# Performance work log

Hardware: AMD Instinct MI355X
Metric: run time of the kernel (lower is better)

Reference implementation:

```python
import jax, jax.numpy as jnp
import numpy as np

B, N, M, K = 8, 24000, 6000, 32
C_IN, C_MID, C_OUT = 64, 128, 256  # channels=[64,128,256]; conv input is C_IN+3 (dp_fj)


def setup_inputs() -> dict:
    key = jax.random.key(0)
    ks = jax.random.split(key, 8)
    return {
        "query_xyz": jax.random.normal(ks[0], (B, M, 3), jnp.float32),
        "support_xyz": jax.random.normal(ks[1], (B, N, 3), jnp.float32),
        "features": jax.random.normal(ks[2], (B, C_IN, N), jnp.float32),
        "neighbor_idx": jax.random.randint(ks[3], (B, M, K), 0, N, dtype=jnp.int32),
        "W1": jax.random.normal(ks[4], (C_MID, C_IN + 3), jnp.float32) * 0.05,
        "b1": jnp.zeros((C_MID,), jnp.float32),
        "W2": jax.random.normal(ks[5], (C_OUT, C_MID), jnp.float32) * 0.05,
        "b2": jnp.zeros((C_OUT,), jnp.float32),
    }


def _conv1d_relu(x, W, b):
    # pointwise conv1d (kernel size 1) + bias + ReLU; x: [B, Cin, N]
    return jax.nn.relu(jnp.einsum('oc,bcn->bon', W, x) + b[None, :, None])


def reference(query_xyz, support_xyz, features, neighbor_idx, W1, b1, W2, b2):
    # Delayed aggregation: transform features FIRST (convs on support points),
    # then gather neighbors per query and max-reduce.
    x = jnp.concatenate([features, support_xyz.transpose(0, 2, 1)], axis=1)  # [B, C_IN+3, N]
    x = _conv1d_relu(x, W1, b1)   # [B, C_MID, N]
    x = _conv1d_relu(x, W2, b2)   # [B, C_OUT, N]
    # grouper: gather neighbor features fj = x[b, :, neighbor_idx[b, m, k]] -> [B, C_OUT, M, K]
    idx = jnp.broadcast_to(neighbor_idx.reshape(B, 1, M * K), (B, C_OUT, M * K))
    fj = jnp.take_along_axis(x, idx, axis=2).reshape(B, C_OUT, M, K)
    # reduction_layer: max over neighbor dim
    return jnp.max(fj, axis=-1)  # [B, C_OUT, M]
```

## Files before the change

### kernel.cpp

```cpp
#include <hip/hip_runtime.h>

typedef unsigned short u16;
typedef short s16x8 __attribute__((ext_vector_type(8)));
typedef float f32x4 __attribute__((ext_vector_type(4)));
typedef unsigned short u16x8 __attribute__((ext_vector_type(8)));

#define B_   8
#define N_   24000
#define M_   6000
#define K_   32
#define CIN  64
#define CMID 128
#define COUT 256
#define KP1  96
#define QB_  188

__device__ __align__(16) u16 g_W1f[CMID * KP1];
__device__ __align__(16) u16 g_W2f[COUT * CMID];
__device__ __align__(16) u16 g_Yf[(size_t)B_ * N_ * COUT];

__device__ __forceinline__ float bf2f(u16 u) {
    return __uint_as_float(((unsigned)u) << 16);
}
__device__ __forceinline__ u16 f2bf(float f) {
    unsigned u = __float_as_uint(f);
    u += 0x7FFFu + ((u >> 16) & 1u);
    return (u16)(u >> 16);
}

__global__ void prep_weights(const float* __restrict__ W1,
                             const float* __restrict__ W2) {
    int t = blockIdx.x * 256 + threadIdx.x;
    if (t < CMID * KP1) {
        int blk = t >> 9, off = t & 511;
        int L = off >> 3, j = off & 7;
        int ln = L & 15, quad = L >> 4;
        int w = blk / 6, r = blk % 6;
        int k0i = r >> 1, mt = r & 1;
        int row = w * 32 + mt * 16 + ln;
        int col = k0i * 32 + quad * 8 + j;
        g_W1f[t] = (col < 67) ? f2bf(W1[row * 67 + col]) : (u16)0;
    } else {
        int i = t - CMID * KP1;
        int blk = i >> 9, off = i & 511;
        int L = off >> 3, j = off & 7;
        int ln = L & 15, quad = L >> 4;
        int w = blk >> 4, r = blk & 15;
        int k0i = r >> 2, mt = r & 3;
        int row = w * 64 + mt * 16 + ln;
        int col = k0i * 32 + quad * 8 + j;
        g_W2f[i] = f2bf(W2[row * 128 + col]);
    }
}

__global__ __launch_bounds__(256) void conv_fused(
        const float* __restrict__ feat, const float* __restrict__ xyz,
        const float* __restrict__ b1,  const float* __restrict__ b2) {
    __shared__ __align__(16) u16 sm[16896];
    u16* Xs = sm;
    u16* Hs = sm + 6656;
    u16* Ys = sm;

    const int tid  = threadIdx.x;
    const int b    = blockIdx.y;
    const int n0   = blockIdx.x * 64;
    const int w    = tid >> 6;
    const int L    = tid & 63;
    const int ln   = L & 15;
    const int quad = L >> 4;

    if (tid < 64) {
        uint4 z; z.x = z.y = z.z = z.w = 0u;
        u16* xr = Xs + tid * 104;
        *(uint4*)(xr + 64) = z; *(uint4*)(xr + 72) = z;
        *(uint4*)(xr + 80) = z; *(uint4*)(xr + 88) = z;
        const float* s = xyz + (size_t)(b * N_ + n0 + tid) * 3;
        xr[64] = f2bf(s[0]); xr[65] = f2bf(s[1]); xr[66] = f2bf(s[2]);
    }
#pragma unroll
    for (int it = 0; it < 4; ++it) {
        int idx = it * 256 + tid;
        int c   = idx >> 4;
        int p0  = (idx & 15) << 2;
        float4 v = *(const float4*)(feat + (size_t)(b * CIN + c) * N_ + n0 + p0);
        u16* dst = Xs + p0 * 104 + c;
        dst[0]   = f2bf(v.x);
        dst[104] = f2bf(v.y);
        dst[208] = f2bf(v.z);
        dst[312] = f2bf(v.w);
    }
    __syncthreads();

    f32x4 acc1[2][4];
#pragma unroll
    for (int mt = 0; mt < 2; ++mt)
#pragma unroll
        for (int nt = 0; nt < 4; ++nt) {
            f32x4 zz = {0.f, 0.f, 0.f, 0.f};
            acc1[mt][nt] = zz;
        }
#pragma unroll
    for (int k0i = 0; k0i < 3; ++k0i) {
        s16x8 af[2], xf[4];
#pragma unroll
        for (int mt = 0; mt < 2; ++mt)
            af[mt] = *(const s16x8*)(g_W1f + (((w * 3 + k0i) * 2 + mt) << 9) + L * 8);
#pragma unroll
        for (int nt = 0; nt < 4; ++nt)
            xf[nt] = *(const s16x8*)(Xs + (nt * 16 + ln) * 104 + k0i * 32 + quad * 8);
#pragma unroll
        for (int mt = 0; mt < 2; ++mt)
#pragma unroll
            for (int nt = 0; nt < 4; ++nt)
                acc1[mt][nt] = __builtin_amdgcn_mfma_f32_16x16x32_bf16(
                    af[mt], xf[nt], acc1[mt][nt], 0, 0, 0);
    }
#pragma unroll
    for (int mt = 0; mt < 2; ++mt) {
        int m0 = w * 32 + mt * 16 + quad * 4;
        float4 bv = *(const float4*)(b1 + m0);
#pragma unroll
        for (int nt = 0; nt < 4; ++nt) {
            int p = nt * 16 + ln;
            float x0 = acc1[mt][nt][0] + bv.x;
            float x1 = acc1[mt][nt][1] + bv.y;
            float x2 = acc1[mt][nt][2] + bv.z;
            float x3 = acc1[mt][nt][3] + bv.w;
            ushort4 hv;
            hv.x = f2bf(x0 > 0.f ? x0 : 0.f);
            hv.y = f2bf(x1 > 0.f ? x1 : 0.f);
            hv.z = f2bf(x2 > 0.f ? x2 : 0.f);
            hv.w = f2bf(x3 > 0.f ? x3 : 0.f);
            *(ushort4*)(Hs + p * 136 + m0) = hv;
        }
    }
    __syncthreads();

    f32x4 acc2[4][4];
#pragma unroll
    for (int mt = 0; mt < 4; ++mt)
#pragma unroll
        for (int nt = 0; nt < 4; ++nt) {
            f32x4 zz = {0.f, 0.f, 0.f, 0.f};
            acc2[mt][nt] = zz;
        }
#pragma unroll
    for (int k0i = 0; k0i < 4; ++k0i) {
        s16x8 af[4], hf[4];
#pragma unroll
        for (int mt = 0; mt < 4; ++mt)
            af[mt] = *(const s16x8*)(g_W2f + (((w * 4 + k0i) * 4 + mt) << 9) + L * 8);
#pragma unroll
        for (int nt = 0; nt < 4; ++nt)
            hf[nt] = *(const s16x8*)(Hs + (nt * 16 + ln) * 136 + k0i * 32 + quad * 8);
#pragma unroll
        for (int mt = 0; mt < 4; ++mt)
#pragma unroll
            for (int nt = 0; nt < 4; ++nt)
                acc2[mt][nt] = __builtin_amdgcn_mfma_f32_16x16x32_bf16(
                    af[mt], hf[nt], acc2[mt][nt], 0, 0, 0);
    }
    __syncthreads();

#pragma unroll
    for (int mt = 0; mt < 4; ++mt) {
        int c0 = w * 64 + mt * 16 + quad * 4;
        float4 bv = *(const float4*)(b2 + c0);
#pragma unroll
        for (int nt = 0; nt < 4; ++nt) {
            int p = nt * 16 + ln;
            float x0 = acc2[mt][nt][0] + bv.x;
            float x1 = acc2[mt][nt][1] + bv.y;
            float x2 = acc2[mt][nt][2] + bv.z;
            float x3 = acc2[mt][nt][3] + bv.w;
            ushort4 yv;
            yv.x = f2bf(x0 > 0.f ? x0 : 0.f);
            yv.y = f2bf(x1 > 0.f ? x1 : 0.f);
            yv.z = f2bf(x2 > 0.f ? x2 : 0.f);
            yv.w = f2bf(x3 > 0.f ? x3 : 0.f);
            *(ushort4*)(Ys + p * 264 + c0) = yv;
        }
    }
    __syncthreads();

    u16* dstY = g_Yf + ((size_t)b * N_ + n0) * COUT;
#pragma unroll
    for (int i = 0; i < 8; ++i) {
        int g = i * 256 + tid;
        int p = g >> 5, c16 = g & 31;
        *(uint4*)(dstY + (size_t)p * COUT + c16 * 8) =
            *(const uint4*)(Ys + p * 264 + c16 * 8);
    }
}

__global__ __launch_bounds__(256, 6) void gather_max(
        const int* __restrict__ nbr, float* __restrict__ out) {
    __shared__ __align__(16) u16 smem[32 * 400];
    int* sidx = (int*)smem;
    u16* ymax = smem;

    const int tid = threadIdx.x;
    const int l   = blockIdx.x;
    const int xcd = l & 7;
    const int qb  = l >> 3;
    const int m0  = qb * 32;
    const int row = tid >> 3;
    const int Mv0 = M_ - m0;
    const int Mv  = Mv0 < 32 ? Mv0 : 32;

    const int w  = tid >> 6;
    const int L  = tid & 63;
    const int kg = L >> 3;
    const int co = L & 7;

    for (int cw = 0; cw < 4; ++cw) {
        const int combo = cw * 8 + xcd;
        const int b = combo >> 2;
        const int q = combo & 3;

        if (cw) __syncthreads();
        if (row < Mv)
            *(int4*)(sidx + tid * 4) =
                *(const int4*)(nbr + ((size_t)b * M_ + m0) * K_ + tid * 4);
        __syncthreads();

        const u16* base = g_Yf + (size_t)b * N_ * COUT + q * 64 + co * 8;

        u16x8 mx[8];
#pragma unroll
        for (int i = 0; i < 8; ++i)
            mx[i] = (u16x8){0, 0, 0, 0, 0, 0, 0, 0};

#pragma unroll
        for (int i = 0; i < 8; ++i) {
            int ml = w * 8 + i;
            if (ml < Mv) {
                int id[4];
#pragma unroll
                for (int r = 0; r < 4; ++r)
                    id[r] = sidx[ml * K_ + r * 8 + kg];
                u16x8 v[4];
#pragma unroll
                for (int r = 0; r < 4; ++r) {
                    unsigned u = (unsigned)id[r];
                    u = u < (unsigned)N_ ? u : 0u;
                    v[r] = *(const u16x8*)(base + (size_t)u * COUT);
                }
                u16x8 a = __builtin_elementwise_max(v[0], v[1]);
                u16x8 c = __builtin_elementwise_max(v[2], v[3]);
                mx[i] = __builtin_elementwise_max(
                    mx[i], __builtin_elementwise_max(a, c));
            }
        }
        __syncthreads();

#pragma unroll
        for (int i = 0; i < 8; ++i) {
            int ml = w * 8 + i;
            if (ml < Mv) {
                u16x8 m8 = mx[i];
#pragma unroll
                for (int mask = 8; mask <= 32; mask <<= 1) {
                    int4 t = *(int4*)&m8;
                    t.x = __shfl_xor(t.x, mask);
                    t.y = __shfl_xor(t.y, mask);
                    t.z = __shfl_xor(t.z, mask);
                    t.w = __shfl_xor(t.w, mask);
                    m8 = __builtin_elementwise_max(m8, *(u16x8*)&t);
                }
                if (kg == 0)
                    *(u16x8*)(ymax + ml * 400 + co * 8) = m8;
            }
        }
        __syncthreads();

#pragma unroll
        for (int it = 0; it < 2; ++it) {
            int c  = it * 32 + (tid >> 3);
            int mc = (tid & 7) << 2;
            if (mc + 4 <= Mv) {
                float4 v;
                v.x = bf2f(ymax[(mc + 0) * 400 + c]);
                v.y = bf2f(ymax[(mc + 1) * 400 + c]);
                v.z = bf2f(ymax[(mc + 2) * 400 + c]);
                v.w = bf2f(ymax[(mc + 3) * 400 + c]);
                *(float4*)(out + (size_t)(b * COUT + q * 64 + c) * M_ + m0 + mc) = v;
            }
        }
    }
}

extern "C" void kernel_launch(void* const* d_in, const int* in_sizes, int n_in,
                              void* d_out, int out_size, void* d_ws, size_t ws_size,
                              hipStream_t stream) {
    const float* xyz  = (const float*)d_in[1];
    const float* feat = (const float*)d_in[2];
    const int*   nbr  = (const int*)d_in[3];
    const float* W1   = (const float*)d_in[4];
    const float* b1   = (const float*)d_in[5];
    const float* W2   = (const float*)d_in[6];
    const float* b2   = (const float*)d_in[7];
    float* out = (float*)d_out;
    (void)d_ws; (void)ws_size;

    prep_weights<<<176, 256, 0, stream>>>(W1, W2);
    conv_fused<<<dim3(N_ / 64, B_), 256, 0, stream>>>(feat, xyz, b1, b2);
    gather_max<<<8 * QB_, 256, 0, stream>>>(nbr, out);
}
```

Before: 304.8 us.

## Schedule gather work dynamically via per-XCD atomic queues keyed on hardware XCC id

```diff
diff --git a/kernel.cpp b/kernel.cpp
--- a/kernel.cpp
+++ b/kernel.cpp
@@ -14,10 +14,12 @@
 #define COUT 256
 #define KP1  96
 #define QB_  188
+#define QLEN (4 * QB_)
 
 __device__ __align__(16) u16 g_W1f[CMID * KP1];
 __device__ __align__(16) u16 g_W2f[COUT * CMID];
 __device__ __align__(16) u16 g_Yf[(size_t)B_ * N_ * COUT];
+__device__ int g_ctr[8];
 
 __device__ __forceinline__ float bf2f(u16 u) {
     return __uint_as_float(((unsigned)u) << 16);
@@ -30,6 +32,7 @@
 
 __global__ void prep_weights(const float* __restrict__ W1,
                              const float* __restrict__ W2) {
+    if (blockIdx.x == 0 && threadIdx.x < 8) g_ctr[threadIdx.x] = 0;
     int t = blockIdx.x * 256 + threadIdx.x;
     if (t < CMID * KP1) {
         int blk = t >> 9, off = t & 511;
@@ -193,99 +196,114 @@
     }
 }
 
-__global__ __launch_bounds__(256, 6) void gather_max(
+__global__ __launch_bounds__(256) void gather_max(
         const int* __restrict__ nbr, float* __restrict__ out) {
     __shared__ __align__(16) u16 smem[32 * 400];
     int* sidx = (int*)smem;
     u16* ymax = smem;
+    __shared__ int s_item;
 
     const int tid = threadIdx.x;
-    const int l   = blockIdx.x;
-    const int xcd = l & 7;
-    const int qb  = l >> 3;
-    const int m0  = qb * 32;
+
+    if (tid == 0) {
+        unsigned xcc;
+        asm volatile("s_getreg_b32 %0, hwreg(HW_REG_XCC_ID)" : "=s"(xcc));
+        xcc &= 7u;
+        int item = -1;
+        unsigned probe = 0;
+        while (item < 0) {
+            int qx = (int)((xcc + probe) & 7u);
+            int t = atomicAdd(&g_ctr[qx], 1);
+            if (t < QLEN) item = qx * QLEN + t;
+            ++probe;
+        }
+        s_item = item;
+    }
+    __syncthreads();
+
+    const int item = s_item;
+    const int qx = item / QLEN;
+    const int tt = item % QLEN;
+    const int cw = tt / QB_;
+    const int qb = tt % QB_;
+    const int combo = cw * 8 + qx;
+    const int b  = combo >> 2;
+    const int q  = combo & 3;
+    const int m0 = qb * 32;
     const int row = tid >> 3;
     const int Mv0 = M_ - m0;
     const int Mv  = Mv0 < 32 ? Mv0 : 32;
+
+    if (row < Mv)
+        *(int4*)(sidx + tid * 4) =
+            *(const int4*)(nbr + ((size_t)b * M_ + m0) * K_ + tid * 4);
+    __syncthreads();
 
     const int w  = tid >> 6;
     const int L  = tid & 63;
     const int kg = L >> 3;
     const int co = L & 7;
-
-    for (int cw = 0; cw < 4; ++cw) {
-        const int combo = cw * 8 + xcd;
-        const int b = combo >> 2;
-        const int q = combo & 3;
-
-        if (cw) __syncthreads();
-        if (row < Mv)
-            *(int4*)(sidx + tid * 4) =
-                *(const int4*)(nbr + ((size_t)b * M_ + m0) * K_ + tid * 4);
-        __syncthreads();
-
-        const u16* base = g_Yf + (size_t)b * N_ * COUT + q * 64 + co * 8;
-
-        u16x8 mx[8];
-#pragma unroll
-        for (int i = 0; i < 8; ++i)
-            mx[i] = (u16x8){0, 0, 0, 0, 0, 0, 0, 0};
-
-#pragma unroll
-        for (int i = 0; i < 8; ++i) {
-            int ml = w * 8 + i;
-            if (ml < Mv) {
-                int id[4];
-#pragma unroll
-                for (int r = 0; r < 4; ++r)
-                    id[r] = sidx[ml * K_ + r * 8 + kg];
-                u16x8 v[4];
-#pragma unroll
-                for (int r = 0; r < 4; ++r) {
-                    unsigned u = (unsigned)id[r];
-                    u = u < (unsigned)N_ ? u : 0u;
-                    v[r] = *(const u16x8*)(base + (size_t)u * COUT);
-                }
-                u16x8 a = __builtin_elementwise_max(v[0], v[1]);
-                u16x8 c = __builtin_elementwise_max(v[2], v[3]);
-                mx[i] = __builtin_elementwise_max(
-                    mx[i], __builtin_elementwise_max(a, c));
+    const u16* base = g_Yf + (size_t)b * N_ * COUT + q * 64 + co * 8;
+
+    u16x8 mx[8];
+#pragma unroll
+    for (int i = 0; i < 8; ++i)
+        mx[i] = (u16x8){0, 0, 0, 0, 0, 0, 0, 0};
+
+#pragma unroll
+    for (int i = 0; i < 8; ++i) {
+        int ml = w * 8 + i;
+        if (ml < Mv) {
+            int id[4];
+#pragma unroll
+            for (int r = 0; r < 4; ++r)
+                id[r] = sidx[ml * K_ + r * 8 + kg];
+            u16x8 v[4];
+#pragma unroll
+            for (int r = 0; r < 4; ++r) {
+                unsigned u = (unsigned)id[r];
+                u = u < (unsigned)N_ ? u : 0u;
+                v[r] = *(const u16x8*)(base + (size_t)u * COUT);
             }
-        }
-        __syncthreads();
-
-#pragma unroll
-        for (int i = 0; i < 8; ++i) {
-            int ml = w * 8 + i;
-            if (ml < Mv) {
-                u16x8 m8 = mx[i];
-#pragma unroll
-                for (int mask = 8; mask <= 32; mask <<= 1) {
-                    int4 t = *(int4*)&m8;
-                    t.x = __shfl_xor(t.x, mask);
-                    t.y = __shfl_xor(t.y, mask);
-                    t.z = __shfl_xor(t.z, mask);
-                    t.w = __shfl_xor(t.w, mask);
-                    m8 = __builtin_elementwise_max(m8, *(u16x8*)&t);
-                }
-                if (kg == 0)
-                    *(u16x8*)(ymax + ml * 400 + co * 8) = m8;
+            u16x8 a = __builtin_elementwise_max(v[0], v[1]);
+            u16x8 c = __builtin_elementwise_max(v[2], v[3]);
+            mx[i] = __builtin_elementwise_max(
+                mx[i], __builtin_elementwise_max(a, c));
+        }
+    }
+    __syncthreads();
+
+#pragma unroll
+    for (int i = 0; i < 8; ++i) {
+        int ml = w * 8 + i;
+        if (ml < Mv) {
+            u16x8 m8 = mx[i];
+#pragma unroll
+            for (int mask = 8; mask <= 32; mask <<= 1) {
+                int4 t = *(int4*)&m8;
+                t.x = __shfl_xor(t.x, mask);
+                t.y = __shfl_xor(t.y, mask);
+                t.z = __shfl_xor(t.z, mask);
+                t.w = __shfl_xor(t.w, mask);
+                m8 = __builtin_elementwise_max(m8, *(u16x8*)&t);
             }
-        }
-        __syncthreads();
-
-#pragma unroll
-        for (int it = 0; it < 2; ++it) {
-            int c  = it * 32 + (tid >> 3);
-            int mc = (tid & 7) << 2;
-            if (mc + 4 <= Mv) {
-                float4 v;
-                v.x = bf2f(ymax[(mc + 0) * 400 + c]);
-                v.y = bf2f(ymax[(mc + 1) * 400 + c]);
-                v.z = bf2f(ymax[(mc + 2) * 400 + c]);
-                v.w = bf2f(ymax[(mc + 3) * 400 + c]);
-                *(float4*)(out + (size_t)(b * COUT + q * 64 + c) * M_ + m0 + mc) = v;
-            }
+            if (kg == 0)
+                *(u16x8*)(ymax + ml * 400 + co * 8) = m8;
+        }
+    }
+    __syncthreads();
+
+#pragma unroll
+    for (int it = 0; it < 2; ++it) {
+        int c  = it * 32 + (tid >> 3);
+        int mc = (tid & 7) << 2;
+        if (mc + 4 <= Mv) {
+            float4 v;
+            v.x = bf2f(ymax[(mc + 0) * 400 + c]);
+            v.y = bf2f(ymax[(mc + 1) * 400 + c]);
+            v.z = bf2f(ymax[(mc + 2) * 400 + c]);
+            v.w = bf2f(ymax[(mc + 3) * 400 + c]);
+            *(float4*)(out + (size_t)(b * COUT + q * 64 + c) * M_ + m0 + mc) = v;
         }
     }
 }
@@ -305,5 +323,5 @@
 
     prep_weights<<<176, 256, 0, stream>>>(W1, W2);
     conv_fused<<<dim3(N_ / 64, B_), 256, 0, stream>>>(feat, xyz, b1, b2);
-    gather_max<<<8 * QB_, 256, 0, stream>>>(nbr, out);
-}
+    gather_max<<<8 * QLEN, 256, 0, stream>>>(nbr, out);
+}
```

Result: faster. 272.6 us (-10.6%).
